# Performance work log

Measured on AMD Instinct MI355X. Metric: run time of the kernel, lower is better.

The kernel has to match this reference:

```python
import jax, jax.numpy as jnp
import numpy as np

D_MODEL = 2048
HEADS = 16
INNER = 8192
SEQ = 2048
BATCH = 1  # source code's mask.reshape(B,1,L,L) requires B==1
EPS = 1e-5


def _layer_norm(x, gamma, beta):
    mu = jnp.mean(x, axis=-1, keepdims=True)
    var = jnp.mean(jnp.square(x - mu), axis=-1, keepdims=True)
    return (x - mu) * jax.lax.rsqrt(var + EPS) * gamma + beta


def setup_inputs() -> dict:
    key = jax.random.key(0)
    ks = jax.random.split(key, 14)
    s = 0.02
    return {
        "x": jax.random.normal(ks[0], (BATCH, SEQ, D_MODEL), jnp.float32),
        # weights stored as (in, out)
        "Wqkv": jax.random.normal(ks[1], (D_MODEL, 3 * D_MODEL), jnp.float32) * s,
        "bqkv": jnp.zeros((3 * D_MODEL,), jnp.float32),
        "Wo": jax.random.normal(ks[2], (D_MODEL, D_MODEL), jnp.float32) * s,
        "bo": jnp.zeros((D_MODEL,), jnp.float32),
        "W1": jax.random.normal(ks[3], (D_MODEL, INNER), jnp.float32) * s,
        "b1": jnp.zeros((INNER,), jnp.float32),
        "W2": jax.random.normal(ks[4], (INNER, D_MODEL), jnp.float32) * s,
        "b2": jnp.zeros((D_MODEL,), jnp.float32),
        "g1": jnp.ones((D_MODEL,), jnp.float32),
        "be1": jnp.zeros((D_MODEL,), jnp.float32),
        "g2": jnp.ones((D_MODEL,), jnp.float32),
        "be2": jnp.zeros((D_MODEL,), jnp.float32),
    }


def reference(x, Wqkv, bqkv, Wo, bo, W1, b1, W2, b2, g1, be1, g2, be2):
    B, L, D = x.shape
    H, hd = HEADS, D // HEADS
    qkv = x @ Wqkv + bqkv                       # [B,L,3D]
    q, k, v = jnp.split(qkv, 3, axis=-1)
    q = q.reshape(B, L, H, hd)
    k = k.reshape(B, L, H, hd)
    v = v.reshape(B, L, H, hd)
    # NOTE: faithful to source, scale is 1/sqrt(D) not 1/sqrt(head_dim)
    scores = jnp.einsum("bqhd,bkhd->bhqk", q, k) / jnp.sqrt(jnp.float32(D))
    causal = jnp.tril(jnp.ones((L, L), bool))   # [L,L] broadcast over B,H
    scores = jnp.where(causal, scores, -jnp.inf)
    attn = jax.nn.softmax(scores, axis=-1)      # dropout = identity (eval)
    out = jnp.einsum("bhqk,bkhd->bqhd", attn, v).reshape(B, L, D)
    lin = out @ Wo + bo
    h = _layer_norm(x + lin, g1, be1)
    ff = jax.nn.gelu(h @ W1 + b1, approximate=False) @ W2 + b2
    return _layer_norm(h + ff, g2, be2)
```

## Files before the change

kernel.cpp:

```cpp
#include <hip/hip_runtime.h>
#include <hip/hip_bf16.h>

typedef unsigned short u16;
typedef __attribute__((ext_vector_type(8))) short frag8;
typedef __attribute__((ext_vector_type(4))) float facc4;

#define L_SEQ 2048
#define D_MODEL 2048
#define N_HEADS 16
#define HEAD_D 128
#define N_QKV 6144
#define D_INNER 8192

__device__ __forceinline__ u16 f2b(float f) {
    __hip_bfloat16 h = __float2bfloat16(f);
    return *reinterpret_cast<u16*>(&h);
}

__device__ __forceinline__ float b2f(u16 u) {
    __hip_bfloat16 h = *reinterpret_cast<__hip_bfloat16*>(&u);
    return __bfloat162float(h);
}

__device__ __forceinline__ void gload_lds16(const void* g, void* l) {
    __builtin_amdgcn_global_load_lds(
        (const __attribute__((address_space(1))) unsigned int*)g,
        (__attribute__((address_space(3))) unsigned int*)l, 16, 0, 0);
}

__device__ __forceinline__ float gelu_exact(float x) {
    return 0.5f * x * (1.0f + erff(x * 0.7071067811865475f));
}

__global__ __launch_bounds__(256) void cvt_bf16_kernel(const float* __restrict__ in, u16* __restrict__ out, int n) {
    const int i = (blockIdx.x * 256 + threadIdx.x) * 8;
    if (i >= n) return;
    float4 a = *(const float4*)(in + i);
    float4 b = *(const float4*)(in + i + 4);
    u16 tmp[8];
    tmp[0] = f2b(a.x); tmp[1] = f2b(a.y); tmp[2] = f2b(a.z); tmp[3] = f2b(a.w);
    tmp[4] = f2b(b.x); tmp[5] = f2b(b.y); tmp[6] = f2b(b.z); tmp[7] = f2b(b.w);
    *(uint4*)(out + i) = *(uint4*)tmp;
}

__global__ __launch_bounds__(256) void tr_cvt64(const float* __restrict__ in, u16* __restrict__ out, int R, int C) {
    __shared__ float t[64][68];
    const int bx = blockIdx.x * 64;
    const int by = blockIdx.y * 64;
    const int tid = threadIdx.x;
    {
        const int r = tid >> 2;
        const int c4 = (tid & 3) * 16;
        const float* src = in + (size_t)(by + r) * C + bx + c4;
#pragma unroll
        for (int j = 0; j < 4; ++j)
            *(float4*)&t[r][c4 + 4 * j] = *(const float4*)(src + 4 * j);
    }
    __syncthreads();
    {
        const int cc = tid >> 2;
        const int rr0 = (tid & 3) * 16;
        u16 tmp[16];
#pragma unroll
        for (int j = 0; j < 16; ++j) tmp[j] = f2b(t[rr0 + j][cc]);
        u16* dst = out + (size_t)(bx + cc) * R + by + rr0;
        *(uint4*)(dst) = *(uint4*)&tmp[0];
        *(uint4*)(dst + 8) = *(uint4*)&tmp[8];
    }
}

__global__ __launch_bounds__(256) void gemm_bt(const u16* __restrict__ A, const u16* __restrict__ Bt,
                                               const float* __restrict__ bias, float* __restrict__ Cout,
                                               int M, int N, int K) {
    __shared__ u16 lA[128 * 64];
    __shared__ u16 lB[128 * 64];
    const int tid = threadIdx.x;
    const int lane = tid & 63, wid = tid >> 6;
    const int wr = wid >> 1, wc = wid & 1;
    const int l15 = lane & 15, g4 = lane >> 4;
    const int bm = blockIdx.y, bn = blockIdx.x;

    const int arow = tid >> 3;
    const int acol = (tid & 7) * 8;
    const size_t abase = (size_t)(bm * 128) * K + acol;
    const size_t bbase = (size_t)(bn * 128) * K + acol;

    facc4 acc[4][4] = {};

    for (int k0 = 0; k0 < K; k0 += 64) {
        if (k0) __syncthreads();
#pragma unroll
        for (int i = 0; i < 4; i++) {
            gload_lds16(A + abase + (size_t)(i * 32 + arow) * K + k0, &lA[i * 2048 + tid * 8]);
            gload_lds16(Bt + bbase + (size_t)(i * 32 + arow) * K + k0, &lB[i * 2048 + tid * 8]);
        }
        __syncthreads();
#pragma unroll
        for (int kk = 0; kk < 64; kk += 32) {
            frag8 af[4], bf[4];
#pragma unroll
            for (int m = 0; m < 4; m++)
                af[m] = *(const frag8*)&lA[(wr * 64 + m * 16 + l15) * 64 + kk + g4 * 8];
#pragma unroll
            for (int n = 0; n < 4; n++)
                bf[n] = *(const frag8*)&lB[(wc * 64 + n * 16 + l15) * 64 + kk + g4 * 8];
#pragma unroll
            for (int m = 0; m < 4; m++)
#pragma unroll
                for (int n = 0; n < 4; n++)
                    acc[m][n] = __builtin_amdgcn_mfma_f32_16x16x32_bf16(af[m], bf[n], acc[m][n], 0, 0, 0);
        }
    }

    const int row0 = bm * 128 + wr * 64 + g4 * 4;
    const int col0 = bn * 128 + wc * 64 + l15;
#pragma unroll
    for (int n = 0; n < 4; n++) {
        const int col = col0 + n * 16;
        const float bv = bias[col];
#pragma unroll
        for (int m = 0; m < 4; m++)
#pragma unroll
            for (int r = 0; r < 4; r++)
                Cout[(size_t)(row0 + m * 16 + r) * N + col] = acc[m][n][r] + bv;
    }
}

template <int EPI>
__global__ __launch_bounds__(512, 2) void gemm256(const u16* __restrict__ A, const u16* __restrict__ Bt,
                                                  const float* __restrict__ bias, void* __restrict__ Cout,
                                                  float* __restrict__ q0, float* __restrict__ q1,
                                                  float* __restrict__ q2, float* __restrict__ q3,
                                                  int M, int N, int K, int kseg, int nbm) {
    __shared__ u16 lds[4 * 16384];
    const int tid = threadIdx.x;
    const int lane = tid & 63, wid = tid >> 6;
    const int wm = wid >> 2, wn = wid & 3;
    const int l15 = lane & 15, g4 = lane >> 4;

    const int nwg = gridDim.x;
    const int q8 = nwg >> 3;
    const int wg = (blockIdx.x & 7) * q8 + (blockIdx.x >> 3);
    const int bm = wg % nbm, bn = wg / nbm;
    const int kb = blockIdx.z * kseg;
    const int ksz = (blockIdx.z == (int)gridDim.z - 1) ? (K - kb) : kseg;
    const int nt = ksz >> 5;

    const int rA = tid >> 2;
    const int swzT = ((tid >> 3) & 3) << 4;
    const int srcE = ((((tid & 3) << 4) ^ swzT) >> 1);
    const u16* Ab = A + (size_t)(bm * 256 + rA) * K + kb + srcE;
    const u16* Bb = Bt + (size_t)(bn * 256 + rA) * K + kb + srcE;
    const size_t rstride = (size_t)128 * K;

    int aoff[8], boff[4];
#pragma unroll
    for (int mf = 0; mf < 8; mf++) {
        const int rowl = wm * 128 + mf * 16 + l15;
        aoff[mf] = rowl * 32 + (((g4 * 16) ^ (((rowl >> 1) & 3) << 4)) >> 1);
    }
#pragma unroll
    for (int nf = 0; nf < 4; nf++) {
        const int rowl = wn * 64 + nf * 16 + l15;
        boff[nf] = rowl * 32 + (((g4 * 16) ^ (((rowl >> 1) & 3) << 4)) >> 1);
    }

    auto stageA = [&](int tt) {
        u16* sA = &lds[(tt & 3) * 16384];
        const u16* g = Ab + (size_t)tt * 32;
        gload_lds16(g, sA + tid * 8);
        gload_lds16(g + rstride, sA + 4096 + tid * 8);
    };
    auto stageB = [&](int tt) {
        u16* sB = &lds[(tt & 3) * 16384 + 8192];
        const u16* g = Bb + (size_t)tt * 32;
        gload_lds16(g, sB + tid * 8);
        gload_lds16(g + rstride, sB + 4096 + tid * 8);
    };

    facc4 acc[8][4] = {};

    stageA(0); stageB(0);
    stageA(1); stageB(1);
    stageA(2); stageB(2);
    asm volatile("s_waitcnt vmcnt(8)" ::: "memory");
    __builtin_amdgcn_s_barrier();
    __builtin_amdgcn_sched_barrier(0);

    for (int t = 0; t < nt; ++t) {
        const u16* sA = &lds[(t & 3) * 16384];
        const u16* sB = sA + 8192;
        frag8 b0[4], ap[2];
#pragma unroll
        for (int i = 0; i < 4; i++) b0[i] = *(const frag8*)&sB[boff[i]];
        ap[0] = *(const frag8*)&sA[aoff[0]];
        ap[1] = *(const frag8*)&sA[aoff[1]];
        if (t + 3 < nt) stageA(t + 3);
        __builtin_amdgcn_s_setprio(1);
#pragma unroll
        for (int m = 0; m < 2; m++)
#pragma unroll
            for (int nf = 0; nf < 4; nf++)
                acc[m][nf] = __builtin_amdgcn_mfma_f32_16x16x32_bf16(ap[m], b0[nf], acc[m][nf], 0, 0, 0);
        __builtin_amdgcn_s_setprio(0);
        ap[0] = *(const frag8*)&sA[aoff[2]];
        ap[1] = *(const frag8*)&sA[aoff[3]];
        __builtin_amdgcn_s_setprio(1);
#pragma unroll
        for (int m = 0; m < 2; m++)
#pragma unroll
            for (int nf = 0; nf < 4; nf++)
                acc[2 + m][nf] = __builtin_amdgcn_mfma_f32_16x16x32_bf16(ap[m], b0[nf], acc[2 + m][nf], 0, 0, 0);
        __builtin_amdgcn_s_setprio(0);
        __builtin_amdgcn_s_barrier();
        ap[0] = *(const frag8*)&sA[aoff[4]];
        ap[1] = *(const frag8*)&sA[aoff[5]];
        if (t + 3 < nt) stageB(t + 3);
        __builtin_amdgcn_s_setprio(1);
#pragma unroll
        for (int m = 0; m < 2; m++)
#pragma unroll
            for (int nf = 0; nf < 4; nf++)
                acc[4 + m][nf] = __builtin_amdgcn_mfma_f32_16x16x32_bf16(ap[m], b0[nf], acc[4 + m][nf], 0, 0, 0);
        __builtin_amdgcn_s_setprio(0);
        ap[0] = *(const frag8*)&sA[aoff[6]];
        ap[1] = *(const frag8*)&sA[aoff[7]];
        __builtin_amdgcn_s_setprio(1);
#pragma unroll
        for (int m = 0; m < 2; m++)
#pragma unroll
            for (int nf = 0; nf < 4; nf++)
                acc[6 + m][nf] = __builtin_amdgcn_mfma_f32_16x16x32_bf16(ap[m], b0[nf], acc[6 + m][nf], 0, 0, 0);
        __builtin_amdgcn_s_setprio(0);
        if (t + 3 < nt)
            asm volatile("s_waitcnt vmcnt(8)" ::: "memory");
        else if (t + 2 < nt)
            asm volatile("s_waitcnt vmcnt(4)" ::: "memory");
        else
            asm volatile("s_waitcnt vmcnt(0)" ::: "memory");
        __builtin_amdgcn_s_barrier();
        __builtin_amdgcn_sched_barrier(0);
    }

    const int row0 = bm * 256 + wm * 128 + g4 * 4;
    const int col0 = bn * 256 + wn * 64 + l15;
    float* fout;
    if (EPI == 3) {
        const int z = blockIdx.z;
        fout = (z == 0) ? q0 : (z == 1) ? q1 : (z == 2) ? q2 : q3;
    } else {
        fout = (float*)Cout;
    }
#pragma unroll
    for (int nf = 0; nf < 4; nf++) {
        const int col = col0 + nf * 16;
        const float bv = (EPI == 3) ? 0.0f : bias[col];
#pragma unroll
        for (int mf = 0; mf < 8; mf++) {
#pragma unroll
            for (int r = 0; r < 4; r++) {
                const int row = row0 + mf * 16 + r;
                float v = acc[mf][nf][r] + bv;
                if (EPI == 2) v = gelu_exact(v);
                if (EPI == 0 || EPI == 3)
                    fout[(size_t)row * N + col] = v;
                else
                    ((u16*)Cout)[(size_t)row * N + col] = f2b(v);
            }
        }
    }
}

__global__ __launch_bounds__(256) void attn_kernel(const u16* __restrict__ qkv, u16* __restrict__ out) {
    __shared__ u16 kT[64 * 128];
    __shared__ u16 vT[128 * 64];
    const int h = blockIdx.y;
    const int qb = (blockIdx.y < 8) ? ((int)gridDim.x - 1 - (int)blockIdx.x) : (int)blockIdx.x;
    const int tid = threadIdx.x;
    const int lane = tid & 63, w = tid >> 6;
    const int l15 = lane & 15, g4 = lane >> 4;
    const int q0 = qb * 64 + w * 16;
    const float scale = 0.022097086912079608f;

    frag8 qf[4];
    {
        const u16* qrow = qkv + (size_t)(q0 + l15) * N_QKV + h * HEAD_D + g4 * 8;
#pragma unroll
        for (int c = 0; c < 4; c++) qf[c] = *(const frag8*)(qrow + c * 32);
    }

    float m_run = -1e30f, l_run = 0.0f;
    facc4 o[8] = {};

    const int src0 = ((g4 & 1) << 5) + l15;
    const int src1 = src0 + 16;
    const bool hi = (g4 & 2) != 0;

    const int nt = qb + 1;
    for (int t = 0; t < nt; ++t) {
        const int kbase = t * 64;
        if (t) __syncthreads();
        const u16* kg_ptr = qkv + (size_t)kbase * N_QKV + D_MODEL + h * HEAD_D;
        const u16* vg_ptr = kg_ptr + D_MODEL;
        uint4 vv[4];
#pragma unroll
        for (int i = 0; i < 4; ++i)
            vv[i] = *(const uint4*)(vg_ptr + (size_t)lane * N_QKV + w * 32 + i * 8);
#pragma unroll
        for (int p = 0; p < 4; ++p) {
            const int c = p * 256 + tid;
            const int row = c >> 4;
            const int colb = (c & 15) << 4;
            const int srcb = colb ^ ((row & 7) << 4);
            gload_lds16(kg_ptr + (size_t)row * N_QKV + (srcb >> 1), &kT[c * 8]);
        }
#pragma unroll
        for (int i = 0; i < 4; ++i) {
            const u16* pv = (const u16*)&vv[i];
#pragma unroll
            for (int e = 0; e < 8; ++e) {
                const int d = w * 32 + i * 8 + e;
                vT[d * 64 + ((((lane >> 3) ^ (d & 7)) << 3) | (lane & 7))] = pv[e];
            }
        }
        __syncthreads();

        const bool last = (t == nt - 1);

        float st[16];
        float mx = -1e30f;
#pragma unroll
        for (int ks = 0; ks < 4; ++ks) {
            const bool active = !last || (ks <= w);
            if (active) {
                facc4 s = {};
                const int kl = ks * 16 + l15;
#pragma unroll
                for (int c = 0; c < 4; ++c) {
                    const int colb = (g4 * 16 + c * 64) ^ ((kl & 7) << 4);
                    frag8 kf = *(const frag8*)&kT[kl * 128 + (colb >> 1)];
                    s = __builtin_amdgcn_mfma_f32_16x16x32_bf16(kf, qf[c], s, 0, 0, 0);
                }
#pragma unroll
                for (int r = 0; r < 4; ++r) {
                    float v = s[r] * scale;
                    if (last) {
                        const int key = kbase + ks * 16 + g4 * 4 + r;
                        if (key > q0 + l15) v = -1e30f;
                    }
                    st[ks * 4 + r] = v;
                    mx = fmaxf(mx, v);
                }
            } else {
#pragma unroll
                for (int r = 0; r < 4; ++r) st[ks * 4 + r] = -1e30f;
            }
        }

        mx = fmaxf(mx, __shfl_xor(mx, 16));
        mx = fmaxf(mx, __shfl_xor(mx, 32));
        const bool skip = __all(mx <= m_run + 8.0f);
        const float m_new = skip ? m_run : fmaxf(m_run, mx);
        const float alpha = __expf(m_run - m_new);
        float ps = 0.0f;
        uint2 pb[4];
#pragma unroll
        for (int ks = 0; ks < 4; ++ks) {
            const float p0 = __expf(st[ks * 4 + 0] - m_new);
            const float p1 = __expf(st[ks * 4 + 1] - m_new);
            const float p2 = __expf(st[ks * 4 + 2] - m_new);
            const float p3 = __expf(st[ks * 4 + 3] - m_new);
            ps += (p0 + p1) + (p2 + p3);
            pb[ks].x = (unsigned)f2b(p0) | ((unsigned)f2b(p1) << 16);
            pb[ks].y = (unsigned)f2b(p2) | ((unsigned)f2b(p3) << 16);
        }
        ps += __shfl_xor(ps, 16);
        ps += __shfl_xor(ps, 32);
        l_run = l_run * alpha + ps;
        m_run = m_new;
        if (!skip) {
#pragma unroll
            for (int c8 = 0; c8 < 8; ++c8)
#pragma unroll
                for (int r = 0; r < 4; ++r) o[c8][r] *= alpha;
        }

#pragma unroll
        for (int kp = 0; kp < 2; ++kp) {
            const bool kp_active = !last || (kp == 0) || (w >= 2);
            if (kp_active) {
                const uint2 a = pb[2 * kp], b = pb[2 * kp + 1];
                const unsigned a0 = __shfl(a.x, src0), a1 = __shfl(a.y, src0);
                const unsigned a2 = __shfl(a.x, src1), a3 = __shfl(a.y, src1);
                const unsigned b0 = __shfl(b.x, src0), b1 = __shfl(b.y, src0);
                const unsigned b2 = __shfl(b.x, src1), b3 = __shfl(b.y, src1);
                union { unsigned u[4]; frag8 f; } pu;
                pu.u[0] = hi ? b0 : a0;
                pu.u[1] = hi ? b1 : a1;
                pu.u[2] = hi ? b2 : a2;
                pu.u[3] = hi ? b3 : a3;
                const frag8 pf = pu.f;
#pragma unroll
                for (int c8 = 0; c8 < 8; ++c8) {
                    const int d = c8 * 16 + l15;
                    const int ch = (((kp * 4 + g4) ^ (l15 & 7)) << 3);
                    frag8 vf = *(const frag8*)&vT[d * 64 + ch];
                    o[c8] = __builtin_amdgcn_mfma_f32_16x16x32_bf16(vf, pf, o[c8], 0, 0, 0);
                }
            }
        }
    }

    const float inv_l = 1.0f / l_run;
    u16* orow = out + (size_t)(q0 + l15) * D_MODEL + h * HEAD_D;
#pragma unroll
    for (int c8 = 0; c8 < 8; ++c8) {
        uint2 st2;
        st2.x = (unsigned)f2b(o[c8][0] * inv_l) | ((unsigned)f2b(o[c8][1] * inv_l) << 16);
        st2.y = (unsigned)f2b(o[c8][2] * inv_l) | ((unsigned)f2b(o[c8][3] * inv_l) << 16);
        *(uint2*)&orow[c8 * 16 + g4 * 4] = st2;
    }
}

__global__ __launch_bounds__(256) void ln_kernel(const float* __restrict__ a, const float* __restrict__ b,
                                                 const float* __restrict__ gamma, const float* __restrict__ beta,
                                                 u16* __restrict__ outb) {
    __shared__ float red[8];
    const int row = blockIdx.x;
    const int tid = threadIdx.x;
    const float* pa = a + (size_t)row * D_MODEL;
    const float* pb = b + (size_t)row * D_MODEL;
    float v[8];
    float s = 0.0f, s2 = 0.0f;
#pragma unroll
    for (int i = 0; i < 8; i++) {
        const int c = tid + i * 256;
        const float x = pa[c] + pb[c];
        v[i] = x;
        s += x;
        s2 += x * x;
    }
#pragma unroll
    for (int off = 32; off; off >>= 1) {
        s += __shfl_xor(s, off);
        s2 += __shfl_xor(s2, off);
    }
    if ((tid & 63) == 0) { red[(tid >> 6) * 2] = s; red[(tid >> 6) * 2 + 1] = s2; }
    __syncthreads();
    s = red[0] + red[2] + red[4] + red[6];
    s2 = red[1] + red[3] + red[5] + red[7];
    const float mean = s * (1.0f / D_MODEL);
    const float var = s2 * (1.0f / D_MODEL) - mean * mean;
    const float rstd = rsqrtf(var + 1e-5f);
#pragma unroll
    for (int i = 0; i < 8; i++) {
        const int c = tid + i * 256;
        outb[(size_t)row * D_MODEL + c] = f2b((v[i] - mean) * rstd * gamma[c] + beta[c]);
    }
}

__global__ __launch_bounds__(256) void ln_part_kernel(const u16* __restrict__ hb,
                                                      const float* __restrict__ p0, const float* __restrict__ p1,
                                                      const float* __restrict__ p2, const float* __restrict__ p3,
                                                      int np, const float* __restrict__ bias,
                                                      const float* __restrict__ gamma, const float* __restrict__ beta,
                                                      float* __restrict__ outf) {
    __shared__ float red[8];
    const int row = blockIdx.x;
    const int tid = threadIdx.x;
    const size_t rb = (size_t)row * D_MODEL;
    float v[8];
    float s = 0.0f, s2 = 0.0f;
#pragma unroll
    for (int i = 0; i < 8; i++) {
        const int c = tid + i * 256;
        float x = b2f(hb[rb + c]) + bias[c] + p0[rb + c] + p1[rb + c];
        if (np > 2) x += p2[rb + c];
        if (np > 3) x += p3[rb + c];
        v[i] = x;
        s += x;
        s2 += x * x;
    }
#pragma unroll
    for (int off = 32; off; off >>= 1) {
        s += __shfl_xor(s, off);
        s2 += __shfl_xor(s2, off);
    }
    if ((tid & 63) == 0) { red[(tid >> 6) * 2] = s; red[(tid >> 6) * 2 + 1] = s2; }
    __syncthreads();
    s = red[0] + red[2] + red[4] + red[6];
    s2 = red[1] + red[3] + red[5] + red[7];
    const float mean = s * (1.0f / D_MODEL);
    const float var = s2 * (1.0f / D_MODEL) - mean * mean;
    const float rstd = rsqrtf(var + 1e-5f);
#pragma unroll
    for (int i = 0; i < 8; i++) {
        const int c = tid + i * 256;
        outf[rb + c] = (v[i] - mean) * rstd * gamma[c] + beta[c];
    }
}

extern "C" void kernel_launch(void* const* d_in, const int* in_sizes, int n_in,
                              void* d_out, int out_size, void* d_ws, size_t ws_size,
                              hipStream_t stream) {
    const float* x    = (const float*)d_in[0];
    const float* Wqkv = (const float*)d_in[1];
    const float* bqkv = (const float*)d_in[2];
    const float* Wo   = (const float*)d_in[3];
    const float* bo   = (const float*)d_in[4];
    const float* W1   = (const float*)d_in[5];
    const float* b1   = (const float*)d_in[6];
    const float* W2   = (const float*)d_in[7];
    const float* b2   = (const float*)d_in[8];
    const float* g1   = (const float*)d_in[9];
    const float* be1  = (const float*)d_in[10];
    const float* g2   = (const float*)d_in[11];
    const float* be2  = (const float*)d_in[12];

    char* ws = (char*)d_ws;
    const size_t MB = 1024 * 1024;
    u16*  xb     = (u16*)(ws + 0);
    u16*  WqkvT  = (u16*)(ws + 8 * MB);
    u16*  qkv    = (u16*)(ws + 32 * MB);
    u16*  attn_o = (u16*)(ws + 56 * MB);
    u16*  WoT    = (u16*)(ws + 8 * MB);
    float* proj  = (float*)(ws + 16 * MB);
    u16*  hb     = (u16*)(ws + 0);
    u16*  W1T    = (u16*)(ws + 8 * MB);
    u16*  f1     = (u16*)(ws + 40 * MB);
    u16*  W2T    = (u16*)(ws + 72 * MB);
    float* part0 = (float*)(ws + 8 * MB);
    float* part1 = (float*)(ws + 24 * MB);
    float* part2 = (float*)(ws + 104 * MB);
    float* part3 = (float*)(ws + 120 * MB);

    const int np = (ws_size >= 136 * MB) ? 4 : 3;
    const int kseg = (np == 4) ? 2048 : 2688;

    cvt_bf16_kernel<<<2048, 256, 0, stream>>>(x, xb, L_SEQ * D_MODEL);
    tr_cvt64<<<dim3(N_QKV / 64, D_MODEL / 64), 256, 0, stream>>>(Wqkv, WqkvT, D_MODEL, N_QKV);
    gemm256<1><<<dim3(192, 1, 1), 512, 0, stream>>>(xb, WqkvT, bqkv, qkv, nullptr, nullptr, nullptr, nullptr,
                                                    L_SEQ, N_QKV, D_MODEL, D_MODEL, 8);
    attn_kernel<<<dim3(L_SEQ / 64, N_HEADS), 256, 0, stream>>>(qkv, attn_o);
    tr_cvt64<<<dim3(D_MODEL / 64, D_MODEL / 64), 256, 0, stream>>>(Wo, WoT, D_MODEL, D_MODEL);
    gemm_bt<<<dim3(D_MODEL / 128, L_SEQ / 128), 256, 0, stream>>>(attn_o, WoT, bo, proj, L_SEQ, D_MODEL, D_MODEL);
    ln_kernel<<<L_SEQ, 256, 0, stream>>>(x, proj, g1, be1, hb);
    tr_cvt64<<<dim3(D_INNER / 64, D_MODEL / 64), 256, 0, stream>>>(W1, W1T, D_MODEL, D_INNER);
    gemm256<2><<<dim3(256, 1, 1), 512, 0, stream>>>(hb, W1T, b1, f1, nullptr, nullptr, nullptr, nullptr,
                                                    L_SEQ, D_INNER, D_MODEL, D_MODEL, 8);
    tr_cvt64<<<dim3(D_MODEL / 64, D_INNER / 64), 256, 0, stream>>>(W2, W2T, D_INNER, D_MODEL);
    gemm256<3><<<dim3(64, 1, np), 512, 0, stream>>>(f1, W2T, nullptr, nullptr, part0, part1, part2, part3,
                                                    L_SEQ, D_MODEL, D_INNER, kseg, 8);
    ln_part_kernel<<<L_SEQ, 256, 0, stream>>>(hb, part0, part1, part2, part3, np, b2, g2, be2, (float*)d_out);
}
```

Baseline: 472.2 us.

## Software-pipeline LDS fragment loads across GEMM k-iterations with extra barriers

Restructures the GEMM main loop so the B fragments and first A fragments for the next k-tile are loaded from LDS during the last MFMA group of the current tile. A-fragment reads are issued one MFMA group ahead, and extra workgroup barriers plus sched_barriers are added around each phase to pin the interleaving. The goal is to hide LDS read latency behind matrix math. In exchange it holds more fragments in registers, which could lower occupancy, and it adds barriers per iteration.

```diff
diff --git a/kernel.cpp b/kernel.cpp
--- a/kernel.cpp
+++ b/kernel.cpp
@@ -187,50 +187,56 @@
     __builtin_amdgcn_s_barrier();
     __builtin_amdgcn_sched_barrier(0);
 
+    frag8 bc[4], bn_[4];
+    frag8 ca0, ca1, ra0, ra1, rb0, rb1, rc0, rc1, na0, na1;
+    {
+        const u16* sA = &lds[0];
+        const u16* sB = sA + 8192;
+#pragma unroll
+        for (int i = 0; i < 4; i++) bc[i] = *(const frag8*)&sB[boff[i]];
+        ca0 = *(const frag8*)&sA[aoff[0]];
+        ca1 = *(const frag8*)&sA[aoff[1]];
+    }
+
     for (int t = 0; t < nt; ++t) {
         const u16* sA = &lds[(t & 3) * 16384];
-        const u16* sB = sA + 8192;
-        frag8 b0[4], ap[2];
-#pragma unroll
-        for (int i = 0; i < 4; i++) b0[i] = *(const frag8*)&sB[boff[i]];
-        ap[0] = *(const frag8*)&sA[aoff[0]];
-        ap[1] = *(const frag8*)&sA[aoff[1]];
+        ra0 = *(const frag8*)&sA[aoff[2]];
+        ra1 = *(const frag8*)&sA[aoff[3]];
+        __builtin_amdgcn_sched_barrier(0);
+        __builtin_amdgcn_s_barrier();
+        __builtin_amdgcn_sched_barrier(0);
+        __builtin_amdgcn_s_setprio(1);
+#pragma unroll
+        for (int nf = 0; nf < 4; nf++) {
+            acc[0][nf] = __builtin_amdgcn_mfma_f32_16x16x32_bf16(ca0, bc[nf], acc[0][nf], 0, 0, 0);
+            acc[1][nf] = __builtin_amdgcn_mfma_f32_16x16x32_bf16(ca1, bc[nf], acc[1][nf], 0, 0, 0);
+        }
+        __builtin_amdgcn_s_setprio(0);
+        rb0 = *(const frag8*)&sA[aoff[4]];
+        rb1 = *(const frag8*)&sA[aoff[5]];
         if (t + 3 < nt) stageA(t + 3);
+        __builtin_amdgcn_sched_barrier(0);
+        __builtin_amdgcn_s_barrier();
+        __builtin_amdgcn_sched_barrier(0);
         __builtin_amdgcn_s_setprio(1);
 #pragma unroll
-        for (int m = 0; m < 2; m++)
-#pragma unroll
-            for (int nf = 0; nf < 4; nf++)
-                acc[m][nf] = __builtin_amdgcn_mfma_f32_16x16x32_bf16(ap[m], b0[nf], acc[m][nf], 0, 0, 0);
+        for (int nf = 0; nf < 4; nf++) {
+            acc[2][nf] = __builtin_amdgcn_mfma_f32_16x16x32_bf16(ra0, bc[nf], acc[2][nf], 0, 0, 0);
+            acc[3][nf] = __builtin_amdgcn_mfma_f32_16x16x32_bf16(ra1, bc[nf], acc[3][nf], 0, 0, 0);
+        }
         __builtin_amdgcn_s_setprio(0);
-        ap[0] = *(const frag8*)&sA[aoff[2]];
-        ap[1] = *(const frag8*)&sA[aoff[3]];
+        rc0 = *(const frag8*)&sA[aoff[6]];
+        rc1 = *(const frag8*)&sA[aoff[7]];
+        if (t + 3 < nt) stageB(t + 3);
+        __builtin_amdgcn_sched_barrier(0);
+        __builtin_amdgcn_s_barrier();
+        __builtin_amdgcn_sched_barrier(0);
         __builtin_amdgcn_s_setprio(1);
 #pragma unroll
-        for (int m = 0; m < 2; m++)
-#pragma unroll
-            for (int nf = 0; nf < 4; nf++)
-                acc[2 + m][nf] = __builtin_amdgcn_mfma_f32_16x16x32_bf16(ap[m], b0[nf], acc[2 + m][nf], 0, 0, 0);
-        __builtin_amdgcn_s_setprio(0);
-        __builtin_amdgcn_s_barrier();
-        ap[0] = *(const frag8*)&sA[aoff[4]];
-        ap[1] = *(const frag8*)&sA[aoff[5]];
-        if (t + 3 < nt) stageB(t + 3);
-        __builtin_amdgcn_s_setprio(1);
-#pragma unroll
-        for (int m = 0; m < 2; m++)
-#pragma unroll
-            for (int nf = 0; nf < 4; nf++)
-                acc[4 + m][nf] = __builtin_amdgcn_mfma_f32_16x16x32_bf16(ap[m], b0[nf], acc[4 + m][nf], 0, 0, 0);
-        __builtin_amdgcn_s_setprio(0);
-        ap[0] = *(const frag8*)&sA[aoff[6]];
-        ap[1] = *(const frag8*)&sA[aoff[7]];
-        __builtin_amdgcn_s_setprio(1);
-#pragma unroll
-        for (int m = 0; m < 2; m++)
-#pragma unroll
-            for (int nf = 0; nf < 4; nf++)
-                acc[6 + m][nf] = __builtin_amdgcn_mfma_f32_16x16x32_bf16(ap[m], b0[nf], acc[6 + m][nf], 0, 0, 0);
+        for (int nf = 0; nf < 4; nf++) {
+            acc[4][nf] = __builtin_amdgcn_mfma_f32_16x16x32_bf16(rb0, bc[nf], acc[4][nf], 0, 0, 0);
+            acc[5][nf] = __builtin_amdgcn_mfma_f32_16x16x32_bf16(rb1, bc[nf], acc[5][nf], 0, 0, 0);
+        }
         __builtin_amdgcn_s_setprio(0);
         if (t + 3 < nt)
             asm volatile("s_waitcnt vmcnt(8)" ::: "memory");
@@ -240,6 +246,27 @@
             asm volatile("s_waitcnt vmcnt(0)" ::: "memory");
         __builtin_amdgcn_s_barrier();
         __builtin_amdgcn_sched_barrier(0);
+        if (t + 1 < nt) {
+            const u16* nA = &lds[((t + 1) & 3) * 16384];
+            const u16* nB = nA + 8192;
+#pragma unroll
+            for (int i = 0; i < 4; i++) bn_[i] = *(const frag8*)&nB[boff[i]];
+            na0 = *(const frag8*)&nA[aoff[0]];
+            na1 = *(const frag8*)&nA[aoff[1]];
+        }
+        __builtin_amdgcn_s_setprio(1);
+#pragma unroll
+        for (int nf = 0; nf < 4; nf++) {
+            acc[6][nf] = __builtin_amdgcn_mfma_f32_16x16x32_bf16(rc0, bc[nf], acc[6][nf], 0, 0, 0);
+            acc[7][nf] = __builtin_amdgcn_mfma_f32_16x16x32_bf16(rc1, bc[nf], acc[7][nf], 0, 0, 0);
+        }
+        __builtin_amdgcn_s_setprio(0);
+        if (t + 1 < nt) {
+#pragma unroll
+            for (int i = 0; i < 4; i++) bc[i] = bn_[i];
+            ca0 = na0;
+            ca1 = na1;
+        }
     }
 
     const int row0 = bm * 256 + wm * 128 + g4 * 4;
```

After: 466.3 us. No clear change (-1.3%).

## Restructure GEMM main loop into BK=64 double-buffered quadrant schedule

Applied to the files above, without the earlier changes.

The 256x256 bf16 GEMM main loop moves from a 4-stage, BK=32 LDS ring to a 2-stage, BK=64 double buffer with a new XOR swizzle on 16-byte chunks. Each K-step is split into four quadrant MFMA phases (A half by B half). Each phase's global-to-LDS loads for the next tile sit between barriers, so memory traffic overlaps compute and the per-K-step loop and barrier overhead is spread over more work. The cost is more barriers per iteration, a shallower prefetch depth, and hand-tuned vmcnt waits that must match the issue order exactly.

```diff
diff --git a/kernel.cpp b/kernel.cpp
--- a/kernel.cpp
+++ b/kernel.cpp
@@ -132,7 +132,7 @@
                                                   float* __restrict__ q0, float* __restrict__ q1,
                                                   float* __restrict__ q2, float* __restrict__ q3,
                                                   int M, int N, int K, int kseg, int nbm) {
-    __shared__ u16 lds[4 * 16384];
+    __shared__ u16 lds[2 * 32768];
     const int tid = threadIdx.x;
     const int lane = tid & 63, wid = tid >> 6;
     const int wm = wid >> 2, wn = wid & 3;
@@ -144,103 +144,106 @@
     const int bm = wg % nbm, bn = wg / nbm;
     const int kb = blockIdx.z * kseg;
     const int ksz = (blockIdx.z == (int)gridDim.z - 1) ? (K - kb) : kseg;
-    const int nt = ksz >> 5;
-
-    const int rA = tid >> 2;
-    const int swzT = ((tid >> 3) & 3) << 4;
-    const int srcE = ((((tid & 3) << 4) ^ swzT) >> 1);
-    const u16* Ab = A + (size_t)(bm * 256 + rA) * K + kb + srcE;
-    const u16* Bb = Bt + (size_t)(bn * 256 + rA) * K + kb + srcE;
-    const size_t rstride = (size_t)128 * K;
-
-    int aoff[8], boff[4];
-#pragma unroll
-    for (int mf = 0; mf < 8; mf++) {
-        const int rowl = wm * 128 + mf * 16 + l15;
-        aoff[mf] = rowl * 32 + (((g4 * 16) ^ (((rowl >> 1) & 3) << 4)) >> 1);
-    }
-#pragma unroll
-    for (int nf = 0; nf < 4; nf++) {
-        const int rowl = wn * 64 + nf * 16 + l15;
-        boff[nf] = rowl * 32 + (((g4 * 16) ^ (((rowl >> 1) & 3) << 4)) >> 1);
-    }
-
-    auto stageA = [&](int tt) {
-        u16* sA = &lds[(tt & 3) * 16384];
-        const u16* g = Ab + (size_t)tt * 32;
-        gload_lds16(g, sA + tid * 8);
-        gload_lds16(g + rstride, sA + 4096 + tid * 8);
+    const int nt = ksz >> 6;
+
+    const int rr = tid >> 3;
+    const int kk8 = tid & 7;
+    const int srcE = (kk8 ^ (rr & 7)) << 3;
+    const u16* aS = A + (size_t)(bm * 256 + rr) * K + kb + srcE;
+    const u16* bS = Bt + (size_t)(bn * 256 + ((rr >> 5) << 6) + (rr & 31)) * K + kb + srcE;
+    const size_t r128 = (size_t)128 * K;
+    const size_t r64 = (size_t)64 * K;
+    const size_t c32 = (size_t)32 * K;
+
+    auto stA = [&](int tt, int h) {
+        u16* d = &lds[((tt & 1) << 15) + (h << 13)];
+        const u16* g = aS + (size_t)tt * 64 + (h ? r64 : 0);
+        gload_lds16(g, d + tid * 8);
+        gload_lds16(g + r128, d + 4096 + tid * 8);
     };
-    auto stageB = [&](int tt) {
-        u16* sB = &lds[(tt & 3) * 16384 + 8192];
-        const u16* g = Bb + (size_t)tt * 32;
-        gload_lds16(g, sB + tid * 8);
-        gload_lds16(g + rstride, sB + 4096 + tid * 8);
+    auto stB = [&](int tt, int h) {
+        u16* d = &lds[((tt & 1) << 15) + 16384 + (h << 13)];
+        const u16* g = bS + (size_t)tt * 64 + (h ? c32 : 0);
+        gload_lds16(g, d + tid * 8);
+        gload_lds16(g + r128, d + 4096 + tid * 8);
     };
 
+    const int ch0 = (g4 ^ (l15 & 7)) << 3;
+    const int ch1 = ch0 ^ 32;
+    const int aRdBase = (wm * 64 + l15) * 64;
+    const int bRdBase = (wn * 32 + l15) * 64;
+
+    frag8 a[4][2], b0[2][2], b1[2][2];
     facc4 acc[8][4] = {};
 
-    stageA(0); stageB(0);
-    stageA(1); stageB(1);
-    stageA(2); stageB(2);
-    asm volatile("s_waitcnt vmcnt(8)" ::: "memory");
-    __builtin_amdgcn_s_barrier();
-    __builtin_amdgcn_sched_barrier(0);
+    auto rdA = [&](int bufo, int mh) {
+#pragma unroll
+        for (int mi = 0; mi < 4; ++mi) {
+            const int base = bufo + mh * 8192 + aRdBase + mi * 1024;
+            a[mi][0] = *(const frag8*)&lds[base + ch0];
+            a[mi][1] = *(const frag8*)&lds[base + ch1];
+        }
+    };
+    auto rdB = [&](int bufo, int nh, frag8(&bb)[2][2]) {
+#pragma unroll
+        for (int ni = 0; ni < 2; ++ni) {
+            const int base = bufo + 16384 + nh * 8192 + bRdBase + ni * 1024;
+            bb[ni][0] = *(const frag8*)&lds[base + ch0];
+            bb[ni][1] = *(const frag8*)&lds[base + ch1];
+        }
+    };
+    auto quad = [&](int mh, int nh, frag8(&bb)[2][2]) {
+        __builtin_amdgcn_s_setprio(1);
+#pragma unroll
+        for (int kh = 0; kh < 2; ++kh)
+#pragma unroll
+            for (int mi = 0; mi < 4; ++mi)
+#pragma unroll
+                for (int ni = 0; ni < 2; ++ni)
+                    acc[mh * 4 + mi][nh * 2 + ni] =
+                        __builtin_amdgcn_mfma_f32_16x16x32_bf16(a[mi][kh], bb[ni][kh],
+                                                                acc[mh * 4 + mi][nh * 2 + ni], 0, 0, 0);
+        __builtin_amdgcn_s_setprio(0);
+    };
+
+#define SB __builtin_amdgcn_sched_barrier(0)
+#define BAR __builtin_amdgcn_s_barrier()
+
+    stA(0, 0); stB(0, 0); stB(0, 1); stA(0, 1);
+    asm volatile("s_waitcnt vmcnt(4)" ::: "memory");
+    BAR; SB;
 
     for (int t = 0; t < nt; ++t) {
-        const u16* sA = &lds[(t & 3) * 16384];
-        const u16* sB = sA + 8192;
-        frag8 b0[4], ap[2];
-#pragma unroll
-        for (int i = 0; i < 4; i++) b0[i] = *(const frag8*)&sB[boff[i]];
-        ap[0] = *(const frag8*)&sA[aoff[0]];
-        ap[1] = *(const frag8*)&sA[aoff[1]];
-        if (t + 3 < nt) stageA(t + 3);
-        __builtin_amdgcn_s_setprio(1);
-#pragma unroll
-        for (int m = 0; m < 2; m++)
-#pragma unroll
-            for (int nf = 0; nf < 4; nf++)
-                acc[m][nf] = __builtin_amdgcn_mfma_f32_16x16x32_bf16(ap[m], b0[nf], acc[m][nf], 0, 0, 0);
-        __builtin_amdgcn_s_setprio(0);
-        ap[0] = *(const frag8*)&sA[aoff[2]];
-        ap[1] = *(const frag8*)&sA[aoff[3]];
-        __builtin_amdgcn_s_setprio(1);
-#pragma unroll
-        for (int m = 0; m < 2; m++)
-#pragma unroll
-            for (int nf = 0; nf < 4; nf++)
-                acc[2 + m][nf] = __builtin_amdgcn_mfma_f32_16x16x32_bf16(ap[m], b0[nf], acc[2 + m][nf], 0, 0, 0);
-        __builtin_amdgcn_s_setprio(0);
-        __builtin_amdgcn_s_barrier();
-        ap[0] = *(const frag8*)&sA[aoff[4]];
-        ap[1] = *(const frag8*)&sA[aoff[5]];
-        if (t + 3 < nt) stageB(t + 3);
-        __builtin_amdgcn_s_setprio(1);
-#pragma unroll
-        for (int m = 0; m < 2; m++)
-#pragma unroll
-            for (int nf = 0; nf < 4; nf++)
-                acc[4 + m][nf] = __builtin_amdgcn_mfma_f32_16x16x32_bf16(ap[m], b0[nf], acc[4 + m][nf], 0, 0, 0);
-        __builtin_amdgcn_s_setprio(0);
-        ap[0] = *(const frag8*)&sA[aoff[6]];
-        ap[1] = *(const frag8*)&sA[aoff[7]];
-        __builtin_amdgcn_s_setprio(1);
-#pragma unroll
-        for (int m = 0; m < 2; m++)
-#pragma unroll
-            for (int nf = 0; nf < 4; nf++)
-                acc[6 + m][nf] = __builtin_amdgcn_mfma_f32_16x16x32_bf16(ap[m], b0[nf], acc[6 + m][nf], 0, 0, 0);
-        __builtin_amdgcn_s_setprio(0);
-        if (t + 3 < nt)
-            asm volatile("s_waitcnt vmcnt(8)" ::: "memory");
-        else if (t + 2 < nt)
-            asm volatile("s_waitcnt vmcnt(4)" ::: "memory");
-        else
-            asm volatile("s_waitcnt vmcnt(0)" ::: "memory");
-        __builtin_amdgcn_s_barrier();
-        __builtin_amdgcn_sched_barrier(0);
-    }
+        const int bufo = (t & 1) << 15;
+        const bool so = (t + 1 < nt);
+        rdA(bufo, 0);
+        rdB(bufo, 0, b0);
+        if (so) stA(t + 1, 0);
+        SB; BAR; SB;
+        quad(0, 0, b0);
+        if (so) asm volatile("s_waitcnt vmcnt(4)" ::: "memory");
+        else    asm volatile("s_waitcnt vmcnt(2)" ::: "memory");
+        BAR; SB;
+        rdB(bufo, 1, b1);
+        if (so) stB(t + 1, 0);
+        SB; BAR; SB;
+        quad(0, 1, b1);
+        if (so) asm volatile("s_waitcnt vmcnt(4)" ::: "memory");
+        else    asm volatile("s_waitcnt vmcnt(0)" ::: "memory");
+        BAR; SB;
+        rdA(bufo, 1);
+        if (so) stB(t + 1, 1);
+        SB; BAR; SB;
+        quad(1, 0, b0);
+        BAR; SB;
+        if (so) stA(t + 1, 1);
+        SB; BAR; SB;
+        quad(1, 1, b1);
+        if (so) asm volatile("s_waitcnt vmcnt(4)" ::: "memory");
+        BAR; SB;
+    }
+#undef SB
+#undef BAR
 
     const int row0 = bm * 256 + wm * 128 + g4 * 4;
     const int col0 = bn * 256 + wn * 64 + l15;
```

Result: no change. 463.7 us (-1.8%).
